# Kernel tuning notes

Measured on AMD Instinct MI355X. Metric: run time of the kernel, lower is better.

Reference implementation:

```python
import jax, jax.numpy as jnp
import numpy as np
import math

N = 50000      # nodes
E = 800000     # edges
IN = 256       # in_dim
HD = 128       # n_hid
T = 3          # num_types
R = 4          # num_relations
NH = 8         # n_heads
DK = HD // NH  # d_k = 16
L = 2          # n_layers
MAXT = 240     # RTE max_len


def _rte_table():
    # Faithful to the torch code (including its precedence: (10000**arange)/n_hid/2,
    # which overflows to inf for large indices -> div_term -> 0).
    pos = jnp.arange(MAXT, dtype=jnp.float32)[:, None]
    div = 1.0 / (10000.0 ** jnp.arange(0.0, HD * 2, 2.0, dtype=jnp.float32) / HD / 2.0)
    emb = jnp.zeros((MAXT, HD * 2), jnp.float32)
    emb = emb.at[:, 0::2].set(jnp.sin(pos * div) / math.sqrt(HD))
    emb = emb.at[:, 1::2].set(jnp.cos(pos * div) / math.sqrt(HD))
    return emb


def setup_inputs() -> dict:
    key = jax.random.key(0)
    ks = jax.random.split(key, 20)
    s = 0.02
    inp = {}
    inp["node_feature"] = jax.random.normal(ks[0], (N, IN), jnp.float32)
    inp["node_type"] = jax.random.randint(ks[1], (N,), 0, T)
    inp["edge_time"] = jax.random.randint(ks[2], (E,), 0, MAXT)
    inp["edge_type"] = jax.random.randint(ks[3], (E,), 0, R)
    inp["edge_index"] = jax.random.randint(ks[4], (2, E), 0, N)
    # adapt layer (per node type)
    inp["adapt_W"] = jax.random.normal(ks[5], (T, IN, HD), jnp.float32) * s
    inp["adapt_b"] = jax.random.normal(ks[6], (T, HD), jnp.float32) * s
    # per-layer, per-type linears (stored as [in,out] so y = x @ W + b)
    inp["Wk"] = jax.random.normal(ks[7], (L, T, HD, HD), jnp.float32) * s
    inp["bk"] = jnp.zeros((L, T, HD), jnp.float32)
    inp["Wq"] = jax.random.normal(ks[8], (L, T, HD, HD), jnp.float32) * s
    inp["bq"] = jnp.zeros((L, T, HD), jnp.float32)
    inp["Wv"] = jax.random.normal(ks[9], (L, T, HD, HD), jnp.float32) * s
    inp["bv"] = jnp.zeros((L, T, HD), jnp.float32)
    inp["Wa"] = jax.random.normal(ks[10], (L, T, HD, HD), jnp.float32) * s
    inp["ba"] = jnp.zeros((L, T, HD), jnp.float32)
    inp["rel_pri"] = jnp.ones((L, T, R, T, NH), jnp.float32)
    glorot = math.sqrt(6.0 / (DK + DK))
    inp["rel_att"] = jax.random.uniform(ks[11], (L, R, NH, DK, DK), jnp.float32, -glorot, glorot)
    inp["rel_msg"] = jax.random.uniform(ks[12], (L, R, NH, DK, DK), jnp.float32, -glorot, glorot)
    inp["skip"] = jnp.ones((L, T), jnp.float32)
    inp["rte_emb"] = _rte_table()                                   # [240, 2*HD], frozen sinusoid
    inp["rte_W"] = jax.random.normal(ks[13], (L, HD * 2, HD), jnp.float32) * s
    inp["rte_b"] = jnp.zeros((L, HD), jnp.float32)
    return inp


def _per_type_linear(x, types, W, b):
    # x:[M,in], types:[M] in [0,T); W:[T,in,out], b:[T,out]
    out = jnp.zeros((x.shape[0], W.shape[-1]), x.dtype)
    for t in range(W.shape[0]):
        out = jnp.where((types == t)[:, None], x @ W[t] + b[t], out)
    return out


def _segment_softmax(s, seg, n):
    # s:[E,H] softmax over edges sharing the same target node
    m = jax.ops.segment_max(s, seg, num_segments=n)
    e = jnp.exp(s - m[seg])
    z = jax.ops.segment_sum(e, seg, num_segments=n)
    return e / z[seg]


def _forward(node_feature, node_type, edge_time, edge_type, edge_index,
             adapt_W, adapt_b, Wk, bk, Wq, bq, Wv, bv, Wa, ba,
             rel_pri, rel_att, rel_msg, skip, rte_emb, rte_W, rte_b):
    src = edge_index[0]  # j (source)
    dst = edge_index[1]  # i (target)
    st = node_type[src]
    tt = node_type[dst]
    rel1h = jax.nn.one_hot(edge_type, R, dtype=node_feature.dtype)  # [E,R]

    x = jnp.tanh(_per_type_linear(node_feature, node_type, adapt_W, adapt_b))  # [N,HD]

    for l in range(L):
        # relative temporal encoding of source features (per edge)
        rte = rte_emb[edge_time] @ rte_W[l] + rte_b[l]          # [E,HD]
        src_vec = x[src] + rte                                   # [E,HD]
        # q is a pure function of target node features -> compute per node, gather
        q_nodes = _per_type_linear(x, node_type, Wq[l], bq[l])   # [N,HD]
        q = q_nodes[dst].reshape(E, NH, DK)
        k = _per_type_linear(src_vec, st, Wk[l], bk[l]).reshape(E, NH, DK)
        v = _per_type_linear(src_vec, st, Wv[l], bv[l]).reshape(E, NH, DK)
        k = jnp.einsum('ehd,er,rhdk->ehk', k, rel1h, rel_att[l])
        v = jnp.einsum('ehd,er,rhdk->ehk', v, rel1h, rel_msg[l])
        pri = rel_pri[l][tt, edge_type, st]                      # [E,NH]
        score = (q * k).sum(-1) * pri / math.sqrt(DK)            # [E,NH]
        att = _segment_softmax(score, dst, N)                    # [E,NH]
        msg = (v * att[..., None]).reshape(E, HD)                # [E,HD]
        aggr = jax.ops.segment_sum(msg, dst, num_segments=N)     # [N,HD]
        aggr = jax.nn.gelu(aggr, approximate=False)
        out = _per_type_linear(aggr, node_type, Wa[l], ba[l])    # [N,HD]
        alpha = jax.nn.sigmoid(skip[l])[node_type][:, None]      # [N,1]
        x = out * alpha + x * (1.0 - alpha)
    return x


def reference(node_feature, node_type, edge_time, edge_type, edge_index,
              adapt_W, adapt_b, Wk, bk, Wq, bq, Wv, bv, Wa, ba,
              rel_pri, rel_att, rel_msg, skip, rte_emb, rte_W, rte_b):
    return _forward(node_feature, node_type, edge_time, edge_type, edge_index,
                    adapt_W, adapt_b, Wk, bk, Wq, bq, Wv, bv, Wa, ba,
                    rel_pri, rel_att, rel_msg, skip, rte_emb, rte_W, rte_b)
```

## Files before the change

kernel.cpp:

```cpp
#include <hip/hip_runtime.h>
#include <cstdint>
#include <cstddef>


namespace {

constexpr int T_N  = 3;
constexpr int R_N  = 4;
constexpr int HD   = 128;
constexpr int IND  = 256;
constexpr int NH   = 8;
constexpr int MAXT = 240;

typedef unsigned short u16;
typedef unsigned int   u32;
typedef _Float16 f16;
typedef __attribute__((ext_vector_type(8))) _Float16 f16x8;
typedef __attribute__((ext_vector_type(4))) float    f32x4;

__global__ void k_fill_all(int* __restrict__ cnt, int* __restrict__ esorted,
                           int* __restrict__ nsorted, int* __restrict__ bcnt,
                           int* __restrict__ ncnt, int nCnt, int nE, int nN) {
  int i = blockIdx.x * 256 + threadIdx.x;
  if (i < nCnt) cnt[i] = 0;
  if (i < nE)  esorted[i] = -1;
  if (i < nN)  nsorted[i] = -1;
  if (i < 16) { bcnt[i] = 0; ncnt[i] = 0; }
}
__global__ void k_hist_all(const int* __restrict__ src, const int* __restrict__ etype,
                           const int* __restrict__ ntype, const int* __restrict__ dst,
                           int* __restrict__ cnt, int* __restrict__ bcnt,
                           int* __restrict__ ncnt, int E, int N) {
  __shared__ int loc12[12];
  __shared__ int loc3[3];
  int tid = threadIdx.x;
  if (tid < 12) loc12[tid] = 0;
  if (tid < 3)  loc3[tid] = 0;
  __syncthreads();
  int i = blockIdx.x * 256 + tid;
  if (i < E) {
    atomicAdd(&cnt[dst[i]], 1);
    int b = ntype[src[i]] * R_N + etype[i];
    atomicAdd(&loc12[b], 1);
  }
  if (i < N) atomicAdd(&loc3[ntype[i]], 1);
  __syncthreads();
  if (tid < 12) atomicAdd(&bcnt[tid], loc12[tid]);
  if (tid < 3)  atomicAdd(&ncnt[tid], loc3[tid]);
}
__global__ void k_scan_a(const int* __restrict__ in, int* __restrict__ out,
                         int* __restrict__ bsums, int n) {
  __shared__ int s[256];
  int gid = blockIdx.x * 256 + threadIdx.x;
  int v = (gid < n) ? in[gid] : 0;
  s[threadIdx.x] = v;
  __syncthreads();
  for (int off = 1; off < 256; off <<= 1) {
    int t = (threadIdx.x >= off) ? s[threadIdx.x - off] : 0;
    __syncthreads();
    s[threadIdx.x] += t;
    __syncthreads();
  }
  if (gid < n) out[gid] = s[threadIdx.x] - v;
  if (threadIdx.x == 255) bsums[blockIdx.x] = s[255];
}
__global__ void k_scan_b(int* __restrict__ bsums, int nb) {
  __shared__ int s[256];
  int v = (threadIdx.x < nb) ? bsums[threadIdx.x] : 0;
  s[threadIdx.x] = v;
  __syncthreads();
  for (int off = 1; off < 256; off <<= 1) {
    int t = (threadIdx.x >= off) ? s[threadIdx.x - off] : 0;
    __syncthreads();
    s[threadIdx.x] += t;
    __syncthreads();
  }
  if (threadIdx.x < nb) bsums[threadIdx.x] = s[threadIdx.x] - v;
}
__global__ void k_scan_c_copy(int* __restrict__ out, const int* __restrict__ bsums,
                              int* __restrict__ cnt, int n, int N) {
  int gid = blockIdx.x * 256 + threadIdx.x;
  if (gid < n) {
    int v = out[gid] + bsums[blockIdx.x];
    out[gid] = v;
    if (gid < N) cnt[gid] = v;
  }
}
__global__ void k_scan_small(const int* __restrict__ bcnt, int* __restrict__ bal,
                             int* __restrict__ bcur, const int* __restrict__ ncnt,
                             int* __restrict__ nal, int* __restrict__ ncur) {
  if (threadIdx.x == 0 && blockIdx.x == 0) {
    int run = 0;
    for (int b = 0; b < 12; b++) {
      bal[b] = run; bcur[b] = run;
      run += (bcnt[b] + 63) & ~63;
    }
    bal[12] = run;
    run = 0;
    for (int t = 0; t < 3; t++) {
      nal[t] = run; ncur[t] = run;
      run += (ncnt[t] + 63) & ~63;
    }
    nal[3] = run;
  }
}
__global__ void k_scatter_all(const int* __restrict__ src, const int* __restrict__ etype,
                              const int* __restrict__ ntype, const int* __restrict__ dst,
                              int* __restrict__ cnt, int* __restrict__ rank,
                              int* __restrict__ bcur, int* __restrict__ esorted,
                              int* __restrict__ ncur, int* __restrict__ nsorted,
                              int E, int N) {
  __shared__ int loc12[12], base12[12];
  __shared__ int loc3[3],  base3[3];
  int tid = threadIdx.x;
  if (tid < 12) loc12[tid] = 0;
  if (tid < 3)  loc3[tid] = 0;
  __syncthreads();
  int i = blockIdx.x * 256 + tid;
  int b = 0, lpos = 0, t = 0, lpos3 = 0;
  if (i < E) {
    rank[i] = atomicAdd(&cnt[dst[i]], 1);
    b = ntype[src[i]] * R_N + etype[i];
    lpos = atomicAdd(&loc12[b], 1);
  }
  if (i < N) {
    t = ntype[i];
    lpos3 = atomicAdd(&loc3[t], 1);
  }
  __syncthreads();
  if (tid < 12) { int c = loc12[tid]; base12[tid] = (c > 0) ? atomicAdd(&bcur[tid], c) : 0; }
  if (tid < 3)  { int c = loc3[tid];  base3[tid]  = (c > 0) ? atomicAdd(&ncur[tid], c) : 0; }
  __syncthreads();
  if (i < E) esorted[base12[b] + lpos] = i;
  if (i < N) nsorted[base3[t] + lpos3] = i;
}

__global__ void k_transp_all(const float* __restrict__ adapt_W,
                             const float* __restrict__ Wq,
                             const float* __restrict__ Wa,
                             u16* __restrict__ adaptWT, u16* __restrict__ WqT,
                             u16* __restrict__ WaT) {
  int c = blockIdx.x;
  int y = blockIdx.y;
  int g = y / T_N, t = y % T_N;
  const float* srcp;
  u16* dstp;
  int Kd;
  if (g == 0) {
    srcp = adapt_W + (size_t)t * IND * HD;
    dstp = adaptWT + (size_t)t * HD * IND;
    Kd = IND;
  } else if (g <= 2) {
    int l = g - 1;
    srcp = Wq + ((size_t)l * T_N + t) * HD * HD;
    dstp = WqT + ((size_t)l * T_N + t) * HD * HD;
    Kd = HD;
  } else {
    int l = g - 3;
    srcp = Wa + ((size_t)l * T_N + t) * HD * HD;
    dstp = WaT + ((size_t)l * T_N + t) * HD * HD;
    Kd = HD;
  }
  for (int k = threadIdx.x; k < Kd; k += blockDim.x)
    dstp[(size_t)c * Kd + k] =
        __builtin_bit_cast(u16, (f16)srcp[(size_t)k * HD + c]);
}

__global__ void k_rte(const float* __restrict__ emb, const float* __restrict__ W,
                      const float* __restrict__ bias, u16* __restrict__ out) {
  int bx = blockIdx.x;
  int l = bx / MAXT, t = bx % MAXT;
  int lane = threadIdx.x;
  __shared__ __align__(16) float s[2 * HD];
  ((float4*)s)[lane] = ((const float4*)(emb + (size_t)t * 2 * HD))[lane];
  __syncthreads();
  const float* Wl = W + (size_t)l * 2 * HD * HD;
  float o0 = bias[l * HD + 2 * lane];
  float o1 = bias[l * HD + 2 * lane + 1];
  #pragma unroll 4
  for (int k = 0; k < 2 * HD; k++) {
    float xv = s[k];
    float2 w = ((const float2*)(Wl + (size_t)k * HD))[lane];
    o0 = fmaf(xv, w.x, o0);
    o1 = fmaf(xv, w.y, o1);
  }
  u32 pk = (u32)__builtin_bit_cast(u16, (f16)o0)
         | ((u32)__builtin_bit_cast(u16, (f16)o1) << 16);
  ((u32*)out)[((size_t)l * MAXT + t) * 64 + lane] = pk;
}

__global__ void k_wcomb(const float* __restrict__ Wk, const float* __restrict__ Wv,
                        const float* __restrict__ bk, const float* __restrict__ bv,
                        const float* __restrict__ Ratt, const float* __restrict__ Rmsg,
                        u16* __restrict__ Wcomb, float* __restrict__ bcomb) {
  int gbc = blockIdx.x;
  int l  = gbc / (12 * 256);
  int bc = gbc % (12 * 256);
  int b  = bc >> 8;
  int c  = bc & 255;
  int st = b >> 2, rt = b & 3;
  int k  = threadIdx.x;
  bool isv = (c >= HD);
  int c0 = isv ? c - HD : c;
  int h  = c0 >> 4, cc = c0 & 15;
  const float* W = (isv ? Wv : Wk) + (((size_t)(l * T_N + st) * HD) + k) * HD + h * 16;
  const float* A = (isv ? Rmsg : Ratt) + (((size_t)(l * R_N + rt) * NH + h) * 16) * 16 + cc;
  float s = 0.f;
  #pragma unroll
  for (int d = 0; d < 16; d++) s = fmaf(W[d], A[d * 16], s);
  Wcomb[(((size_t)l * 12 + b) * 256 + c) * HD + k] = __builtin_bit_cast(u16, (f16)s);
  if (k == 0) {
    const float* bb = (isv ? bv : bk) + (size_t)(l * T_N + st) * HD + h * 16;
    float sb = 0.f;
    #pragma unroll
    for (int d = 0; d < 16; d++) sb = fmaf(bb[d], A[d * 16], sb);
    bcomb[((size_t)l * 12 + b) * 256 + c] = sb;
  }
}

template<int K, int ACT, bool AHALF>
__global__ __launch_bounds__(256) void k_ngemm(
    const float* __restrict__ Af, const u16* __restrict__ Ah,
    const u16* __restrict__ WT, const float* __restrict__ bias,
    const int* __restrict__ nsorted, const int* __restrict__ nal,
    const float* __restrict__ skip_l,
    float* __restrict__ out_f, u16* __restrict__ out_h,
    const float* __restrict__ xin) {
  int tile0 = blockIdx.x * 64;
  if (tile0 >= nal[3]) return;
  int t = 0;
  #pragma unroll
  for (int i = 1; i < 3; i++) t += (tile0 >= nal[i]);

  __shared__ __align__(16) u16 ab[64 * K];
  __shared__ int s_nid[64];
  int tid = threadIdx.x;
  int lane = tid & 63, w = tid >> 6;
  int l15 = lane & 15, l4 = lane >> 4;

  if (tid < 64) s_nid[tid] = nsorted[tile0 + tid];
  __syncthreads();

  {
    int r = tid >> 2, q4 = tid & 3;
    int nid = s_nid[r];
    char* rowp = (char*)ab + r * (2 * K);
    int sw = (r & 7) << 4;
    int base = q4 * (K / 2);
    if (nid >= 0) {
      if (AHALF) {
        const f16x8* ap = (const f16x8*)(Ah + (size_t)nid * K + q4 * (K / 4));
        #pragma unroll
        for (int i = 0; i < K / 32; i++)
          *(f16x8*)(rowp + ((base + 16 * i) ^ sw)) = ap[i];
      } else {
        const float4* ap = (const float4*)(Af + (size_t)nid * K + q4 * (K / 4));
        #pragma unroll
        for (int i = 0; i < K / 32; i++) {
          float4 a = ap[2 * i], a2 = ap[2 * i + 1];
          f16x8 hv;
          hv[0] = (f16)a.x;  hv[1] = (f16)a.y;  hv[2] = (f16)a.z;  hv[3] = (f16)a.w;
          hv[4] = (f16)a2.x; hv[5] = (f16)a2.y; hv[6] = (f16)a2.z; hv[7] = (f16)a2.w;
          *(f16x8*)(rowp + ((base + 16 * i) ^ sw)) = hv;
        }
      }
    } else {
      f16x8 z;
      #pragma unroll
      for (int j = 0; j < 8; j++) z[j] = (f16)0.f;
      #pragma unroll
      for (int i = 0; i < K / 32; i++)
        *(f16x8*)(rowp + ((base + 16 * i) ^ sw)) = z;
    }
  }
  __syncthreads();

  f32x4 acc[4][2];
  #pragma unroll
  for (int ni = 0; ni < 2; ni++) {
    float bc = bias[t * HD + w * 32 + ni * 16 + l15];
    #pragma unroll
    for (int mi = 0; mi < 4; mi++) {
      acc[mi][ni][0] = bc; acc[mi][ni][1] = bc;
      acc[mi][ni][2] = bc; acc[mi][ni][3] = bc;
    }
  }
  const u16* Wt = WT + (size_t)t * HD * K;
  #pragma unroll
  for (int ks = 0; ks < K / 32; ks++) {
    int k0 = ks * 32 + 8 * l4;
    f16x8 bf[2], af[4];
    #pragma unroll
    for (int ni = 0; ni < 2; ni++)
      bf[ni] = *(const f16x8*)(Wt + (size_t)(w * 32 + ni * 16 + l15) * K + k0);
    #pragma unroll
    for (int mi = 0; mi < 4; mi++) {
      int row = mi * 16 + l15;
      af[mi] = *(const f16x8*)((const char*)ab + row * (2 * K) +
                               ((2 * k0) ^ ((row & 7) << 4)));
    }
    #pragma unroll
    for (int mi = 0; mi < 4; mi++)
      #pragma unroll
      for (int ni = 0; ni < 2; ni++)
        acc[mi][ni] = __builtin_amdgcn_mfma_f32_16x16x32_f16(af[mi], bf[ni],
                                                             acc[mi][ni], 0, 0, 0);
  }

  float alpha = 0.f;
  if (ACT == 2) alpha = 1.f / (1.f + expf(-skip_l[t]));
  #pragma unroll
  for (int mi = 0; mi < 4; mi++)
    #pragma unroll
    for (int r = 0; r < 4; r++) {
      int rowl = mi * 16 + l4 * 4 + r;
      int nid = s_nid[rowl];
      if (nid >= 0) {
        #pragma unroll
        for (int ni = 0; ni < 2; ni++) {
          int c = w * 32 + ni * 16 + l15;
          float val = acc[mi][ni][r];
          if (ACT == 0) val = tanhf(val);
          if (ACT == 2) {
            float xo = xin[(size_t)nid * HD + c];
            val = val * alpha + xo * (1.f - alpha);
          }
          if (out_f) out_f[(size_t)nid * HD + c] = val;
          if (out_h) out_h[(size_t)nid * HD + c] =
              __builtin_bit_cast(u16, (f16)val);
        }
      }
    }
}

__global__ __launch_bounds__(512) void k_edge_gemm(
    const u16* __restrict__ x_h, const u16* __restrict__ rte_h,
    const u16* __restrict__ Wcomb, const float* __restrict__ bcomb,
    const u16* __restrict__ q_h, const int* __restrict__ esorted,
    const int* __restrict__ bal, const int* __restrict__ src,
    const int* __restrict__ dst, const int* __restrict__ etime,
    const int* __restrict__ ntype, const int* __restrict__ rank,
    const float* __restrict__ pri_l,
    u16* __restrict__ score_h, u16* __restrict__ v_csr) {
  int tile0 = blockIdx.x * 64;
  if (tile0 >= bal[12]) return;
  int b = 0;
  #pragma unroll
  for (int i = 1; i < 12; i++) b += (tile0 >= bal[i]);
  int st = b >> 2, rt = b & 3;

  __shared__ __align__(16) u16 albuf[64 * HD];
  __shared__ int s_eid[64];
  __shared__ int s_dst[64];
  __shared__ int s_rank[64];
  int tid = threadIdx.x;
  int lane = tid & 63, w = tid >> 6;
  int l15 = lane & 15, l4 = lane >> 4;

  if (tid < 64) {
    int e = esorted[tile0 + tid];
    s_eid[tid] = e;
    s_dst[tid] = (e >= 0) ? dst[e] : 0;
    s_rank[tid] = (e >= 0) ? rank[e] : 0;
  }
  __syncthreads();

  {
    int r = tid >> 3, p = tid & 7;
    int e = s_eid[r];
    char* rowp = (char*)albuf + r * 256;
    int sw = (r & 7) << 4;
    if (e >= 0) {
      const f16x8* xs = (const f16x8*)(x_h + (size_t)src[e] * HD + p * 16);
      const f16x8* rp = (const f16x8*)(rte_h + (size_t)etime[e] * HD + p * 16);
      f16x8 h0 = xs[0] + rp[0];
      f16x8 h1 = xs[1] + rp[1];
      *(f16x8*)(rowp + ((p * 32) ^ sw))      = h0;
      *(f16x8*)(rowp + ((p * 32 + 16) ^ sw)) = h1;
    } else {
      f16x8 z;
      #pragma unroll
      for (int j = 0; j < 8; j++) z[j] = (f16)0.f;
      *(f16x8*)(rowp + ((p * 32) ^ sw))      = z;
      *(f16x8*)(rowp + ((p * 32 + 16) ^ sw)) = z;
    }
  }
  __syncthreads();

  f32x4 acc[4][2];
  #pragma unroll
  for (int ni = 0; ni < 2; ni++) {
    float bc = bcomb[b * 256 + w * 32 + ni * 16 + l15];
    #pragma unroll
    for (int mi = 0; mi < 4; mi++) {
      acc[mi][ni][0] = bc; acc[mi][ni][1] = bc;
      acc[mi][ni][2] = bc; acc[mi][ni][3] = bc;
    }
  }
  const u16* Wb = Wcomb + (size_t)b * 256 * HD;
  #pragma unroll
  for (int ks = 0; ks < 4; ks++) {
    int k0 = ks * 32 + 8 * l4;
    f16x8 bf[2], af[4];
    #pragma unroll
    for (int ni = 0; ni < 2; ni++)
      bf[ni] = *(const f16x8*)(Wb + (size_t)(w * 32 + ni * 16 + l15) * HD + k0);
    #pragma unroll
    for (int mi = 0; mi < 4; mi++) {
      int row = mi * 16 + l15;
      af[mi] = *(const f16x8*)((const char*)albuf + row * 256 +
                               ((2 * k0) ^ ((row & 7) << 4)));
    }
    #pragma unroll
    for (int mi = 0; mi < 4; mi++)
      #pragma unroll
      for (int ni = 0; ni < 2; ni++)
        acc[mi][ni] = __builtin_amdgcn_mfma_f32_16x16x32_f16(af[mi], bf[ni],
                                                             acc[mi][ni], 0, 0, 0);
  }
  __syncthreads();

  if (w < 4) {
    #pragma unroll
    for (int mi = 0; mi < 4; mi++)
      #pragma unroll
      for (int r = 0; r < 4; r++) {
        int row = mi * 16 + l4 * 4 + r;
        char* rowp = (char*)albuf + row * 256;
        int sw = (row & 7) << 4;
        #pragma unroll
        for (int ni = 0; ni < 2; ni++) {
          int c = w * 32 + ni * 16 + l15;
          *(u16*)(rowp + ((2 * c) ^ sw)) =
              __builtin_bit_cast(u16, (f16)acc[mi][ni][r]);
        }
      }
  } else {
    int wv = w - 4;
    #pragma unroll
    for (int mi = 0; mi < 4; mi++)
      #pragma unroll
      for (int r = 0; r < 4; r++) {
        int rowl = mi * 16 + l4 * 4 + r;
        if (s_eid[rowl] >= 0) {
          u16* vp = v_csr + (size_t)s_rank[rowl] * HD + wv * 32 + l15;
          #pragma unroll
          for (int ni = 0; ni < 2; ni++)
            vp[ni * 16] = __builtin_bit_cast(u16, (f16)acc[mi][ni][r]);
        }
      }
  }
  __syncthreads();

  {
    int e = tid >> 3, h = tid & 7;
    if (s_eid[e] >= 0) {
      int d = s_dst[e];
      int tt = ntype[d];
      const char* rowp = (const char*)albuf + e * 256;
      int sw = (e & 7) << 4;
      f16x8 kh0 = *(const f16x8*)(rowp + ((h * 32) ^ sw));
      f16x8 kh1 = *(const f16x8*)(rowp + ((h * 32 + 16) ^ sw));
      const f16x8* qp = (const f16x8*)(q_h + (size_t)d * HD + h * 16);
      f16x8 qa = qp[0], qb = qp[1];
      float sc = 0.f;
      #pragma unroll
      for (int j = 0; j < 8; j++) sc += (float)qa[j] * (float)kh0[j];
      #pragma unroll
      for (int j = 0; j < 8; j++) sc += (float)qb[j] * (float)kh1[j];
      float pri = pri_l[((tt * R_N + rt) * T_N + st) * NH + h];
      score_h[(size_t)s_rank[e] * NH + h] =
          __builtin_bit_cast(u16, (f16)(sc * pri * 0.25f));
    }
  }
}

__global__ void k_aggr(const int* __restrict__ row_ptr,
                       const u16* __restrict__ score_h,
                       const u16* __restrict__ v_csr,
                       u16* __restrict__ g_h, int N) {
  int n = blockIdx.x;
  int lane = threadIdx.x;
  int start = row_ptr[n], end = row_ptr[n + 1];

  int h = lane & 7, jj = lane >> 3;
  float m = -3.0e38f;
  for (int idx = start + jj; idx < end; idx += 8)
    m = fmaxf(m, (float)__builtin_bit_cast(f16, score_h[(size_t)idx * NH + h]));
  #pragma unroll
  for (int off = 8; off < 64; off <<= 1) m = fmaxf(m, __shfl_xor(m, off));
  float z = 0.f;
  for (int idx = start + jj; idx < end; idx += 8)
    z += expf((float)__builtin_bit_cast(f16, score_h[(size_t)idx * NH + h]) - m);
  #pragma unroll
  for (int off = 8; off < 64; off <<= 1) z += __shfl_xor(z, off);

  int myh = lane >> 3;
  float md = __shfl(m, myh);
  float zd = __shfl(z, myh);
  float rz = (zd > 0.f) ? 1.f / zd : 0.f;

  float a0 = 0.f, a1 = 0.f;
  for (int idx = start; idx < end; idx++) {
    float sc = (float)__builtin_bit_cast(f16, score_h[(size_t)idx * NH + myh]);
    float wgt = expf(sc - md) * rz;
    u32 v2 = ((const u32*)(v_csr + (size_t)idx * HD))[lane];
    float v0 = (float)__builtin_bit_cast(f16, (u16)(v2 & 0xffffu));
    float v1 = (float)__builtin_bit_cast(f16, (u16)(v2 >> 16));
    a0 = fmaf(wgt, v0, a0);
    a1 = fmaf(wgt, v1, a1);
  }

  a0 = 0.5f * a0 * (1.f + erff(a0 * 0.7071067811865475f));
  a1 = 0.5f * a1 * (1.f + erff(a1 * 0.7071067811865475f));
  u32 pk = (u32)__builtin_bit_cast(u16, (f16)a0)
         | ((u32)__builtin_bit_cast(u16, (f16)a1) << 16);
  ((u32*)(g_h + (size_t)n * HD))[lane] = pk;
}

}

extern "C" void kernel_launch(void* const* d_in, const int* in_sizes, int n_in,
                              void* d_out, int out_size, void* d_ws, size_t ws_size,
                              hipStream_t stream) {
  const float* node_feature = (const float*)d_in[0];
  const int*   node_type    = (const int*)d_in[1];
  const int*   edge_time    = (const int*)d_in[2];
  const int*   edge_type    = (const int*)d_in[3];
  const int*   edge_index   = (const int*)d_in[4];
  const float* adapt_W      = (const float*)d_in[5];
  const float* adapt_b      = (const float*)d_in[6];
  const float* Wk           = (const float*)d_in[7];
  const float* bk           = (const float*)d_in[8];
  const float* Wq           = (const float*)d_in[9];
  const float* bq           = (const float*)d_in[10];
  const float* Wv           = (const float*)d_in[11];
  const float* bv           = (const float*)d_in[12];
  const float* Wa           = (const float*)d_in[13];
  const float* ba           = (const float*)d_in[14];
  const float* rel_pri      = (const float*)d_in[15];
  const float* rel_att      = (const float*)d_in[16];
  const float* rel_msg      = (const float*)d_in[17];
  const float* skip         = (const float*)d_in[18];
  const float* rte_emb      = (const float*)d_in[19];
  const float* rte_W        = (const float*)d_in[20];
  const float* rte_b        = (const float*)d_in[21];

  const int N = in_sizes[1];
  const int E = in_sizes[2];
  const int* src  = edge_index;
  const int* dstp = edge_index + E;

  float* x = (float*)d_out;

  size_t off = 0;
  auto carve = [&](size_t bytes) -> void* {
    void* p = (char*)d_ws + off;
    off += (bytes + 255) & ~(size_t)255;
    return p;
  };
  u16*   v_csr   = (u16*)  carve((size_t)E * HD * 2);
  u16*   score_h = (u16*)  carve((size_t)E * NH * 2);
  u16*   x_h     = (u16*)  carve((size_t)N * HD * 2);
  u16*   qg      = (u16*)  carve((size_t)N * HD * 2);
  u16*   rte_h   = (u16*)  carve((size_t)2 * MAXT * HD * 2);
  u16*   Wcomb   = (u16*)  carve((size_t)2 * 12 * 256 * HD * 2);
  float* bcomb   = (float*)carve((size_t)2 * 12 * 256 * 4);
  u16*   adaptWT = (u16*)  carve((size_t)T_N * HD * IND * 2);
  u16*   WqT     = (u16*)  carve((size_t)2 * T_N * HD * HD * 2);
  u16*   WaT     = (u16*)  carve((size_t)2 * T_N * HD * HD * 2);
  int*   row_ptr = (int*)  carve((size_t)(N + 1) * 4);
  int*   cnt     = (int*)  carve((size_t)(N + 1) * 4);
  int*   rank    = (int*)  carve((size_t)E * 4);
  int*   bsums   = (int*)  carve(1024 * 4);
  int*   bcnt    = (int*)  carve(16 * 4);
  int*   bal     = (int*)  carve(16 * 4);
  int*   bcur    = (int*)  carve(16 * 4);
  int*   ncnt    = (int*)  carve(16 * 4);
  int*   nal     = (int*)  carve(16 * 4);
  int*   ncur    = (int*)  carve(16 * 4);
  const int EP = E + 12 * 64;
  const int NP = N + 3 * 64;
  int*   esorted = (int*)  carve((size_t)EP * 4);
  int*   nsorted = (int*)  carve((size_t)NP * 4);
  (void)ws_size; (void)n_in; (void)out_size;

  const int gE  = (E + 255) / 256;
  const int gN1 = (N + 1 + 255) / 256;
  const int gEP = (EP + 255) / 256;
  const int etiles = (EP + 63) / 64;
  const int ntiles = (NP + 63) / 64;

  k_fill_all<<<gEP, 256, 0, stream>>>(cnt, esorted, nsorted, bcnt, ncnt,
                                      N + 1, EP, NP);
  k_hist_all<<<gE, 256, 0, stream>>>(src, edge_type, node_type, dstp,
                                     cnt, bcnt, ncnt, E, N);
  k_scan_a<<<gN1, 256, 0, stream>>>(cnt, row_ptr, bsums, N + 1);
  k_scan_b<<<1, 256, 0, stream>>>(bsums, gN1);
  k_scan_c_copy<<<gN1, 256, 0, stream>>>(row_ptr, bsums, cnt, N + 1, N);
  k_scan_small<<<1, 64, 0, stream>>>(bcnt, bal, bcur, ncnt, nal, ncur);
  k_scatter_all<<<gE, 256, 0, stream>>>(src, edge_type, node_type, dstp,
                                        cnt, rank, bcur, esorted,
                                        ncur, nsorted, E, N);

  k_transp_all<<<dim3(HD, T_N * 5), 128, 0, stream>>>(adapt_W, Wq, Wa,
                                                      adaptWT, WqT, WaT);
  k_rte<<<2 * MAXT, 64, 0, stream>>>(rte_emb, rte_W, rte_b, rte_h);
  k_wcomb<<<2 * 12 * 256, 128, 0, stream>>>(Wk, Wv, bk, bv, rel_att, rel_msg,
                                            Wcomb, bcomb);

  k_ngemm<IND, 0, false><<<ntiles, 256, 0, stream>>>(
      node_feature, nullptr, adaptWT, adapt_b, nsorted, nal, nullptr,
      x, x_h, nullptr);

  for (int l = 0; l < 2; l++) {
    k_ngemm<HD, 1, true><<<ntiles, 256, 0, stream>>>(
        nullptr, x_h, WqT + (size_t)l * T_N * HD * HD, bq + (size_t)l * T_N * HD,
        nsorted, nal, nullptr, nullptr, qg, nullptr);
    k_edge_gemm<<<etiles, 512, 0, stream>>>(
        x_h, rte_h + (size_t)l * MAXT * HD,
        Wcomb + (size_t)l * 12 * 256 * HD, bcomb + (size_t)l * 12 * 256,
        qg, esorted, bal, src, dstp, edge_time, node_type, rank,
        rel_pri + (size_t)l * T_N * R_N * T_N * NH, score_h, v_csr);
    k_aggr<<<N, 64, 0, stream>>>(row_ptr, score_h, v_csr, qg, N);
    k_ngemm<HD, 2, true><<<ntiles, 256, 0, stream>>>(
        nullptr, qg, WaT + (size_t)l * T_N * HD * HD, ba + (size_t)l * T_N * HD,
        nsorted, nal, skip + (size_t)l * T_N, x, x_h, x);
  }
}
```

Baseline: 801.4 us.

## Fuse Q projection into preceding node GEMM epilogue and pack aggregation blocks

Adds a QF template path to the node GEMM: once the main result is computed, it writes the fp16 output tile into shared memory and immediately runs the next layer's Q projection against it, which removes the separate Q GEMM launches and the re-read of x_h. The layer loop is unrolled so the adapt GEMM produces layer-0 Q and the layer-0 output GEMM produces layer-1 Q. The last output GEMM skips writing the unused fp16 copy. k_aggr now packs four nodes per 256-thread block instead of one node per 64-thread block, cutting block-scheduling overhead. The cost is an extra sync and a second MFMA pass per tile in the fused kernels, with more register pressure. In the adapt GEMM (K=256) the Q pass reads only the first 128 columns of each shared row, so the row stride and swizzle must match what was written.

Result: no change. 799.6 us (-0.2%).

```diff
diff --git a/kernel.cpp b/kernel.cpp
--- a/kernel.cpp
+++ b/kernel.cpp
@@ -218,14 +218,16 @@
   }
 }
 
-template<int K, int ACT, bool AHALF>
+template<int K, int ACT, bool AHALF, bool QF>
 __global__ __launch_bounds__(256) void k_ngemm(
     const float* __restrict__ Af, const u16* __restrict__ Ah,
     const u16* __restrict__ WT, const float* __restrict__ bias,
     const int* __restrict__ nsorted, const int* __restrict__ nal,
     const float* __restrict__ skip_l,
     float* __restrict__ out_f, u16* __restrict__ out_h,
-    const float* __restrict__ xin) {
+    const float* __restrict__ xin,
+    const u16* __restrict__ WT2, const float* __restrict__ bias2,
+    u16* __restrict__ q_out) {
   int tile0 = blockIdx.x * 64;
   if (tile0 >= nal[3]) return;
   int t = 0;
@@ -309,28 +311,84 @@
 
   float alpha = 0.f;
   if (ACT == 2) alpha = 1.f / (1.f + expf(-skip_l[t]));
+  if (QF) __syncthreads();
   #pragma unroll
   for (int mi = 0; mi < 4; mi++)
     #pragma unroll
     for (int r = 0; r < 4; r++) {
       int rowl = mi * 16 + l4 * 4 + r;
       int nid = s_nid[rowl];
-      if (nid >= 0) {
-        #pragma unroll
-        for (int ni = 0; ni < 2; ni++) {
-          int c = w * 32 + ni * 16 + l15;
-          float val = acc[mi][ni][r];
-          if (ACT == 0) val = tanhf(val);
-          if (ACT == 2) {
-            float xo = xin[(size_t)nid * HD + c];
-            val = val * alpha + xo * (1.f - alpha);
-          }
+      #pragma unroll
+      for (int ni = 0; ni < 2; ni++) {
+        int c = w * 32 + ni * 16 + l15;
+        float val = acc[mi][ni][r];
+        if (ACT == 0) val = tanhf(val);
+        if (ACT == 2 && nid >= 0) {
+          float xo = xin[(size_t)nid * HD + c];
+          val = val * alpha + xo * (1.f - alpha);
+        }
+        u16 hb = __builtin_bit_cast(u16, (f16)val);
+        if (nid >= 0) {
           if (out_f) out_f[(size_t)nid * HD + c] = val;
-          if (out_h) out_h[(size_t)nid * HD + c] =
-              __builtin_bit_cast(u16, (f16)val);
+          if (out_h) out_h[(size_t)nid * HD + c] = hb;
+        }
+        if (QF) {
+          char* rowp = (char*)ab + rowl * 256;
+          int sw = (rowl & 7) << 4;
+          *(u16*)(rowp + ((2 * c) ^ sw)) = hb;
         }
       }
     }
+
+  if (QF) {
+    __syncthreads();
+    f32x4 acc2[4][2];
+    #pragma unroll
+    for (int ni = 0; ni < 2; ni++) {
+      float bc = bias2[t * HD + w * 32 + ni * 16 + l15];
+      #pragma unroll
+      for (int mi = 0; mi < 4; mi++) {
+        acc2[mi][ni][0] = bc; acc2[mi][ni][1] = bc;
+        acc2[mi][ni][2] = bc; acc2[mi][ni][3] = bc;
+      }
+    }
+    const u16* Wt2 = WT2 + (size_t)t * HD * HD;
+    #pragma unroll
+    for (int ks = 0; ks < 4; ks++) {
+      int k0 = ks * 32 + 8 * l4;
+      f16x8 bf[2], af[4];
+      #pragma unroll
+      for (int ni = 0; ni < 2; ni++)
+        bf[ni] = *(const f16x8*)(Wt2 + (size_t)(w * 32 + ni * 16 + l15) * HD + k0);
+      #pragma unroll
+      for (int mi = 0; mi < 4; mi++) {
+        int row = mi * 16 + l15;
+        af[mi] = *(const f16x8*)((const char*)ab + row * 256 +
+                                 ((2 * k0) ^ ((row & 7) << 4)));
+      }
+      #pragma unroll
+      for (int mi = 0; mi < 4; mi++)
+        #pragma unroll
+        for (int ni = 0; ni < 2; ni++)
+          acc2[mi][ni] = __builtin_amdgcn_mfma_f32_16x16x32_f16(af[mi], bf[ni],
+                                                                acc2[mi][ni], 0, 0, 0);
+    }
+    #pragma unroll
+    for (int mi = 0; mi < 4; mi++)
+      #pragma unroll
+      for (int r = 0; r < 4; r++) {
+        int rowl = mi * 16 + l4 * 4 + r;
+        int nid = s_nid[rowl];
+        if (nid >= 0) {
+          #pragma unroll
+          for (int ni = 0; ni < 2; ni++) {
+            int c = w * 32 + ni * 16 + l15;
+            q_out[(size_t)nid * HD + c] =
+                __builtin_bit_cast(u16, (f16)acc2[mi][ni][r]);
+          }
+        }
+      }
+  }
 }
 
 __global__ __launch_bounds__(512) void k_edge_gemm(
@@ -479,8 +537,9 @@
                        const u16* __restrict__ score_h,
                        const u16* __restrict__ v_csr,
                        u16* __restrict__ g_h, int N) {
-  int n = blockIdx.x;
-  int lane = threadIdx.x;
+  int n = blockIdx.x * 4 + (threadIdx.x >> 6);
+  if (n >= N) return;
+  int lane = threadIdx.x & 63;
   int start = row_ptr[n], end = row_ptr[n + 1];
 
   int h = lane & 7, jj = lane >> 3;
@@ -590,6 +649,7 @@
   const int gEP = (EP + 255) / 256;
   const int etiles = (EP + 63) / 64;
   const int ntiles = (NP + 63) / 64;
+  const int gAggr  = (N + 3) / 4;
 
   k_fill_all<<<gEP, 256, 0, stream>>>(cnt, esorted, nsorted, bcnt, ncnt,
                                       N + 1, EP, NP);
@@ -609,22 +669,25 @@
   k_wcomb<<<2 * 12 * 256, 128, 0, stream>>>(Wk, Wv, bk, bv, rel_att, rel_msg,
                                             Wcomb, bcomb);
 
-  k_ngemm<IND, 0, false><<<ntiles, 256, 0, stream>>>(
+  k_ngemm<IND, 0, false, true><<<ntiles, 256, 0, stream>>>(
       node_feature, nullptr, adaptWT, adapt_b, nsorted, nal, nullptr,
-      x, x_h, nullptr);
-
-  for (int l = 0; l < 2; l++) {
-    k_ngemm<HD, 1, true><<<ntiles, 256, 0, stream>>>(
-        nullptr, x_h, WqT + (size_t)l * T_N * HD * HD, bq + (size_t)l * T_N * HD,
-        nsorted, nal, nullptr, nullptr, qg, nullptr);
-    k_edge_gemm<<<etiles, 512, 0, stream>>>(
-        x_h, rte_h + (size_t)l * MAXT * HD,
-        Wcomb + (size_t)l * 12 * 256 * HD, bcomb + (size_t)l * 12 * 256,
-        qg, esorted, bal, src, dstp, edge_time, node_type, rank,
-        rel_pri + (size_t)l * T_N * R_N * T_N * NH, score_h, v_csr);
-    k_aggr<<<N, 64, 0, stream>>>(row_ptr, score_h, v_csr, qg, N);
-    k_ngemm<HD, 2, true><<<ntiles, 256, 0, stream>>>(
-        nullptr, qg, WaT + (size_t)l * T_N * HD * HD, ba + (size_t)l * T_N * HD,
-        nsorted, nal, skip + (size_t)l * T_N, x, x_h, x);
-  }
-}
+      x, x_h, nullptr, WqT, bq, qg);
+
+  k_edge_gemm<<<etiles, 512, 0, stream>>>(
+      x_h, rte_h, Wcomb, bcomb, qg, esorted, bal, src, dstp, edge_time,
+      node_type, rank, rel_pri, score_h, v_csr);
+  k_aggr<<<gAggr, 256, 0, stream>>>(row_ptr, score_h, v_csr, qg, N);
+  k_ngemm<HD, 2, true, true><<<ntiles, 256, 0, stream>>>(
+      nullptr, qg, WaT, ba, nsorted, nal, skip,
+      x, x_h, x, WqT + (size_t)T_N * HD * HD, bq + (size_t)T_N * HD, qg);
+
+  k_edge_gemm<<<etiles, 512, 0, stream>>>(
+      x_h, rte_h + (size_t)MAXT * HD,
+      Wcomb + (size_t)12 * 256 * HD, bcomb + (size_t)12 * 256,
+      qg, esorted, bal, src, dstp, edge_time, node_type, rank,
+      rel_pri + (size_t)T_N * R_N * T_N * NH, score_h, v_csr);
+  k_aggr<<<gAggr, 256, 0, stream>>>(row_ptr, score_h, v_csr, qg, N);
+  k_ngemm<HD, 2, true, false><<<ntiles, 256, 0, stream>>>(
+      nullptr, qg, WaT + (size_t)T_N * HD * HD, ba + (size_t)T_N * HD,
+      nsorted, nal, skip + T_N, x, nullptr, x, nullptr, nullptr, nullptr);
+}
```
